# Kernel tuning notes

Hardware: AMD Instinct MI355X
Metric: run time of the kernel (lower is better)

Reference implementation:

```python
import jax, jax.numpy as jnp
import numpy as np

N_NODES = 100000
N_EDGES = 1600000
NODE_FEATURES = 6
H_EMBED = 64
D = 32
OUT_DIM = 1


def _mlp(x, W1, b1, W2, b2):
    h = jnp.tanh(x @ W1 + b1)
    return jnp.tanh(h @ W2 + b2)


def _gcn_conv(h, W, b, src, dst, n_nodes):
    # PyG GCNConv: linear (no bias) -> add self-loops -> sym-normalized scatter-add -> +bias
    hw = h @ W  # [N, D]
    loop = jnp.arange(n_nodes, dtype=src.dtype)
    row = jnp.concatenate([src, loop])  # sources
    col = jnp.concatenate([dst, loop])  # targets
    ones = jnp.ones(row.shape[0], dtype=hw.dtype)
    deg = jax.ops.segment_sum(ones, col, num_segments=n_nodes)
    dinv = jnp.where(deg > 0, jax.lax.rsqrt(deg), 0.0)
    norm = dinv[row] * dinv[col]  # [E+N]
    msg = hw[row] * norm[:, None]  # gather + scale
    out = jax.ops.segment_sum(msg, col, num_segments=n_nodes)
    return out + b


def setup_inputs() -> dict:
    key = jax.random.key(0)
    ks = jax.random.split(key, 16)
    x = jax.random.normal(ks[0], (N_NODES, NODE_FEATURES), dtype=jnp.float32)
    edge_index = jax.random.randint(ks[1], (2, N_EDGES), 0, N_NODES, dtype=jnp.int64)

    def lin(k, din, dout):
        bound = 1.0 / np.sqrt(din)
        kw, kb = jax.random.split(k)
        W = jax.random.uniform(kw, (din, dout), minval=-bound, maxval=bound, dtype=jnp.float32)
        b = jax.random.uniform(kb, (dout,), minval=-bound, maxval=bound, dtype=jnp.float32)
        return W, b

    We1, be1 = lin(ks[2], NODE_FEATURES, H_EMBED)
    We2, be2 = lin(ks[3], H_EMBED, D)
    Wg1, bg1 = lin(ks[4], D, D)
    Wg2, bg2 = lin(ks[5], D, D)
    Wp1, bp1 = lin(ks[6], D, D)
    Wp2, bp2 = lin(ks[7], D, OUT_DIM)
    return {
        "x": x, "edge_index": edge_index,
        "We1": We1, "be1": be1, "We2": We2, "be2": be2,
        "Wg1": Wg1, "bg1": bg1, "Wg2": Wg2, "bg2": bg2,
        "Wp1": Wp1, "bp1": bp1, "Wp2": Wp2, "bp2": bp2,
    }


def reference(x, edge_index, We1, be1, We2, be2, Wg1, bg1, Wg2, bg2, Wp1, bp1, Wp2, bp2):
    n = x.shape[0]
    src, dst = edge_index[0], edge_index[1]
    h = _mlp(x, We1, be1, We2, be2)            # [N, 32]
    h = jax.nn.relu(_gcn_conv(h, Wg1, bg1, src, dst, n))  # dropout = identity (eval)
    h = jax.nn.relu(_gcn_conv(h, Wg2, bg2, src, dst, n))
    return _mlp(h, Wp1, bp1, Wp2, bp2)         # [N, 1]
```

## Files before the change

kernel.cpp:

```cpp
#include <hip/hip_runtime.h>
#include <hip/hip_fp16.h>

#define NN 100000
#define NE 1600000
#define NPB 128
#define NBUCK ((NN + NPB - 1) / NPB)
#define CAP 4096
#define PBLOCKS 128
#define PTPB 1024
#define EPB (NE / PBLOCKS)
#define DUMMY 100000u
#define SENT 0xFFFFFFFFu
#define GBLK 2048
#define GWAVES (GBLK * 4)

__global__ __launch_bounds__(PTPB) void part_kernel(const int* __restrict__ src,
                                                    const int* __restrict__ dst,
                                                    unsigned int* __restrict__ bcount,
                                                    unsigned int* __restrict__ packed) {
    __shared__ unsigned int lcnt[NBUCK];
    __shared__ unsigned int lcur[NBUCK];
    __shared__ unsigned int lend[NBUCK];
    for (int i = threadIdx.x; i < NBUCK; i += PTPB) lcnt[i] = 0u;
    __syncthreads();
    int e0 = blockIdx.x * EPB;
    for (int e = e0 + threadIdx.x; e < e0 + EPB; e += PTPB)
        atomicAdd(&lcnt[((unsigned)dst[e]) >> 7], 1u);
    __syncthreads();
    for (int i = threadIdx.x; i < NBUCK; i += PTPB) {
        unsigned int c = lcnt[i];
        unsigned int rc = (c + 15u) & ~15u;
        unsigned int base = rc ? atomicAdd(&bcount[i], rc) : 0u;
        lcur[i] = base;
        lend[i] = base + rc;
    }
    __syncthreads();
    for (int e = e0 + threadIdx.x; e < e0 + EPB; e += PTPB) {
        unsigned int d = (unsigned)dst[e];
        unsigned int b = d >> 7;
        unsigned int pos = atomicAdd(&lcur[b], 1u);
        packed[(size_t)b * CAP + pos] = ((d & 127u) << 17) | (unsigned)src[e];
    }
    __syncthreads();
    for (int i = threadIdx.x; i < NBUCK; i += PTPB)
        for (unsigned int j = lcur[i]; j < lend[i]; j++)
            packed[(size_t)i * CAP + j] = SENT;
}

__global__ __launch_bounds__(256) void sort_kernel(const unsigned int* __restrict__ bcount,
                                                   unsigned int* __restrict__ packed,
                                                   unsigned int* __restrict__ rsd,
                                                   float* __restrict__ dinv) {
    __shared__ unsigned int lraw[CAP];
    __shared__ unsigned int lsort[CAP];
    __shared__ unsigned int cnt[NPB];
    __shared__ unsigned int ps[NPB];
    __shared__ unsigned int cur[NPB];
    __shared__ unsigned int ntot;
    int b = blockIdx.x;
    int tid = threadIdx.x;
    if (tid < NPB) cnt[tid] = 0u;
    __syncthreads();
    unsigned int n = bcount[b];
    unsigned int* pk = packed + (size_t)b * CAP;
    for (unsigned int i = tid; i < n; i += 256) {
        unsigned int p = pk[i];
        lraw[i] = p;
        if (p != SENT) atomicAdd(&cnt[p >> 17], 1u);
    }
    __syncthreads();
    if (tid < NPB) ps[tid] = (cnt[tid] + 15u) & ~15u;
    __syncthreads();
    for (int off = 1; off < NPB; off <<= 1) {
        unsigned int t = (tid < NPB && tid >= off) ? ps[tid - off] : 0u;
        __syncthreads();
        if (tid < NPB) ps[tid] += t;
        __syncthreads();
    }
    if (tid == NPB - 1) ntot = ps[NPB - 1];
    __syncthreads();
    unsigned int np = ntot;
    for (unsigned int i = tid; i < np; i += 256) lsort[i] = DUMMY;
    if (tid < NPB) cur[tid] = ps[tid] - ((cnt[tid] + 15u) & ~15u);
    __syncthreads();
    for (unsigned int i = tid; i < n; i += 256) {
        unsigned int p = lraw[i];
        if (p != SENT) {
            unsigned int pos = atomicAdd(&cur[p >> 17], 1u);
            lsort[pos] = p & 0x1FFFFu;
        }
    }
    __syncthreads();
    for (unsigned int i = tid; i < np; i += 256) pk[i] = lsort[i];
    if (tid < NPB) {
        int node = b * NPB + tid;
        if (node < NN) {
            unsigned int c = cnt[tid];
            unsigned int pc = (c + 15u) & ~15u;
            unsigned int rs = (unsigned int)(b * CAP) + ps[tid] - pc;
            rsd[node] = rs | ((pc >> 4) << 22);
            dinv[node] = rsqrtf((float)c + 1.0f);
        }
    }
}

__global__ __launch_bounds__(256) void embed_kernel(
    const float* __restrict__ x, const float* __restrict__ We1, const float* __restrict__ be1,
    const float* __restrict__ We2, const float* __restrict__ be2, const float* __restrict__ Wg1,
    const float* __restrict__ dinv, __half* __restrict__ hws1, __half* __restrict__ hws2) {
    __shared__ float sWe1[6 * 64];
    __shared__ float sbe1[64];
    __shared__ float sWe2[64 * 32];
    __shared__ float sbe2[32];
    __shared__ float sWg1[32 * 32];
    for (int i = threadIdx.x; i < 6 * 64; i += 256) sWe1[i] = We1[i];
    for (int i = threadIdx.x; i < 64; i += 256) sbe1[i] = be1[i];
    for (int i = threadIdx.x; i < 64 * 32; i += 256) sWe2[i] = We2[i];
    for (int i = threadIdx.x; i < 32; i += 256) sbe2[i] = be2[i];
    for (int i = threadIdx.x; i < 32 * 32; i += 256) sWg1[i] = Wg1[i];
    __syncthreads();

    int node = blockIdx.x * 256 + threadIdx.x;
    if (node > NN) return;
    if (node == NN) {
        for (int j = 0; j < 32; j++) {
            hws1[(size_t)NN * 32 + j] = __float2half(0.f);
            hws2[(size_t)NN * 32 + j] = __float2half(0.f);
        }
        return;
    }

    float xv[6];
#pragma unroll
    for (int k = 0; k < 6; k++) xv[k] = x[node * 6 + k];

    float h1[64];
#pragma unroll
    for (int j = 0; j < 64; j++) {
        float a = sbe1[j];
#pragma unroll
        for (int k = 0; k < 6; k++) a += xv[k] * sWe1[k * 64 + j];
        h1[j] = tanhf(a);
    }

    float h[32];
#pragma unroll 4
    for (int j = 0; j < 32; j++) {
        float a = sbe2[j];
#pragma unroll
        for (int k = 0; k < 64; k++) a += h1[k] * sWe2[k * 32 + j];
        h[j] = tanhf(a);
    }

    float di = dinv[node];
    __half* o = hws1 + (size_t)node * 32;
#pragma unroll 4
    for (int j = 0; j < 32; j++) {
        float a = 0.f;
#pragma unroll
        for (int k = 0; k < 32; k++) a += h[k] * sWg1[k * 32 + j];
        o[j] = __float2half(a * di);
    }
}

__global__ __launch_bounds__(256) void gather1_kernel(
    const unsigned int* __restrict__ sorted, const unsigned int* __restrict__ rsd,
    const float* __restrict__ dinv, const __half* __restrict__ hws1,
    const float* __restrict__ bg1, const float* __restrict__ Wg2,
    __half* __restrict__ hws2) {
    int lane = threadIdx.x & 63;
    int g = lane >> 4;
    int p = lane & 15;
    int f = lane & 31;
    float wreg[32];
#pragma unroll
    for (int k = 0; k < 32; k++) wreg[k] = Wg2[k * 32 + f];
    float bf = bg1[f];
    int wave = (blockIdx.x * 256 + threadIdx.x) >> 6;
    const __half2* H = (const __half2*)hws1;
    for (int node = wave; node < NN; node += GWAVES) {
        unsigned int r = rsd[node];
        unsigned int base = r & 0x3FFFFFu;
        unsigned int d = (r >> 22) << 4;
        float ax = 0.f, ay = 0.f;
        for (unsigned int k = g; k < d; k += 16) {
            unsigned int s0 = sorted[base + k];
            unsigned int s1 = sorted[base + k + 4];
            unsigned int s2 = sorted[base + k + 8];
            unsigned int s3 = sorted[base + k + 12];
            float2 v0 = __half22float2(H[(size_t)s0 * 16 + p]);
            float2 v1 = __half22float2(H[(size_t)s1 * 16 + p]);
            float2 v2 = __half22float2(H[(size_t)s2 * 16 + p]);
            float2 v3 = __half22float2(H[(size_t)s3 * 16 + p]);
            ax += (v0.x + v1.x) + (v2.x + v3.x);
            ay += (v0.y + v1.y) + (v2.y + v3.y);
        }
        ax += __shfl_xor(ax, 16); ay += __shfl_xor(ay, 16);
        ax += __shfl_xor(ax, 32); ay += __shfl_xor(ay, 32);
        float2 sv = __half22float2(H[(size_t)node * 16 + p]);
        ax += sv.x; ay += sv.y;
        float ae = __shfl(ax, f >> 1);
        float ao = __shfl(ay, f >> 1);
        float av = (f & 1) ? ao : ae;
        float di = dinv[node];
        float h = di * av + bf;
        h = h > 0.f ? h : 0.f;
        float o = 0.f;
#pragma unroll
        for (int k = 0; k < 32; k++) o += __shfl(h, k) * wreg[k];
        if (lane < 32) hws2[(size_t)node * 32 + f] = __float2half(o * di);
    }
}

__global__ __launch_bounds__(256) void gather2_kernel(
    const unsigned int* __restrict__ sorted, const unsigned int* __restrict__ rsd,
    const float* __restrict__ dinv, const __half* __restrict__ hws2,
    const float* __restrict__ bg2, const float* __restrict__ Wp1,
    const float* __restrict__ bp1, const float* __restrict__ Wp2,
    const float* __restrict__ bp2, float* __restrict__ out) {
    int lane = threadIdx.x & 63;
    int g = lane >> 4;
    int p = lane & 15;
    int f = lane & 31;
    float wreg[32];
#pragma unroll
    for (int k = 0; k < 32; k++) wreg[k] = Wp1[k * 32 + f];
    float bgf = bg2[f];
    float b1f = bp1[f];
    float w2f = Wp2[f];
    float b2 = bp2[0];
    int wave = (blockIdx.x * 256 + threadIdx.x) >> 6;
    const __half2* H = (const __half2*)hws2;
    for (int node = wave; node < NN; node += GWAVES) {
        unsigned int r = rsd[node];
        unsigned int base = r & 0x3FFFFFu;
        unsigned int d = (r >> 22) << 4;
        float ax = 0.f, ay = 0.f;
        for (unsigned int k = g; k < d; k += 16) {
            unsigned int s0 = sorted[base + k];
            unsigned int s1 = sorted[base + k + 4];
            unsigned int s2 = sorted[base + k + 8];
            unsigned int s3 = sorted[base + k + 12];
            float2 v0 = __half22float2(H[(size_t)s0 * 16 + p]);
            float2 v1 = __half22float2(H[(size_t)s1 * 16 + p]);
            float2 v2 = __half22float2(H[(size_t)s2 * 16 + p]);
            float2 v3 = __half22float2(H[(size_t)s3 * 16 + p]);
            ax += (v0.x + v1.x) + (v2.x + v3.x);
            ay += (v0.y + v1.y) + (v2.y + v3.y);
        }
        ax += __shfl_xor(ax, 16); ay += __shfl_xor(ay, 16);
        ax += __shfl_xor(ax, 32); ay += __shfl_xor(ay, 32);
        float2 sv = __half22float2(H[(size_t)node * 16 + p]);
        ax += sv.x; ay += sv.y;
        float ae = __shfl(ax, f >> 1);
        float ao = __shfl(ay, f >> 1);
        float av = (f & 1) ? ao : ae;
        float di = dinv[node];
        float h = di * av + bgf;
        h = h > 0.f ? h : 0.f;
        float pre = b1f;
#pragma unroll
        for (int k = 0; k < 32; k++) pre += __shfl(h, k) * wreg[k];
        float t = tanhf(pre) * w2f;
#pragma unroll
        for (int off = 1; off < 32; off <<= 1) t += __shfl_xor(t, off);
        if (lane == 0) out[node] = tanhf(t + b2);
    }
}

extern "C" void kernel_launch(void* const* d_in, const int* in_sizes, int n_in,
                              void* d_out, int out_size, void* d_ws, size_t ws_size,
                              hipStream_t stream) {
    const float* x = (const float*)d_in[0];
    const int* edge = (const int*)d_in[1];
    const int* src = edge;
    const int* dst = edge + NE;
    const float* We1 = (const float*)d_in[2];
    const float* be1 = (const float*)d_in[3];
    const float* We2 = (const float*)d_in[4];
    const float* be2 = (const float*)d_in[5];
    const float* Wg1 = (const float*)d_in[6];
    const float* bg1 = (const float*)d_in[7];
    const float* Wg2 = (const float*)d_in[8];
    const float* bg2 = (const float*)d_in[9];
    const float* Wp1 = (const float*)d_in[10];
    const float* bp1 = (const float*)d_in[11];
    const float* Wp2 = (const float*)d_in[12];
    const float* bp2 = (const float*)d_in[13];
    float* out = (float*)d_out;

    unsigned int* bcount = (unsigned int*)d_ws;
    float* dinv = (float*)d_ws + 1024;
    unsigned int* rsd = (unsigned int*)d_ws + 1024 + NN;
    unsigned int* packed = (unsigned int*)d_ws + 1024 + 2 * NN;
    __half* hws1 = (__half*)((unsigned int*)d_ws + 1024 + 2 * NN + NBUCK * CAP);
    __half* hws2 = hws1 + (size_t)(NN + 1) * 32;

    hipMemsetAsync(bcount, 0, 1024 * sizeof(unsigned int), stream);

    int gridN = (NN + 256) / 256;

    part_kernel<<<PBLOCKS, PTPB, 0, stream>>>(src, dst, bcount, packed);
    sort_kernel<<<NBUCK, 256, 0, stream>>>(bcount, packed, rsd, dinv);
    embed_kernel<<<gridN, 256, 0, stream>>>(x, We1, be1, We2, be2, Wg1, dinv, hws1, hws2);
    gather1_kernel<<<GBLK, 256, 0, stream>>>(packed, rsd, dinv, hws1, bg1, Wg2, hws2);
    gather2_kernel<<<GBLK, 256, 0, stream>>>(packed, rsd, dinv, hws2, bg2, Wp1, bp1, Wp2, bp2, out);
}
```

Before: 278.9 us.

## Map each node to a half-wave and reduce neighbor padding to eight

Each 64-lane wave now serves two nodes: every 32-lane half-wave handles one node's aggregation and the dense 32x32 transform. Per-node neighbor lists are padded to multiples of 8 instead of 16, so fewer dummy rows are gathered. Neighbor indices are loaded four at a time with one uint4 load. Partition and sort block counts, thread counts and the bucket capacity are retuned to fit. In exchange, each node has less memory-level parallelism per gather, the shuffles now use width 32, and the packed buffer needs more workspace.

Measured after the change: 246.0 us. 11.8% less time.

```diff
diff --git a/kernel.cpp b/kernel.cpp
--- a/kernel.cpp
+++ b/kernel.cpp
@@ -5,14 +5,14 @@
 #define NE 1600000
 #define NPB 128
 #define NBUCK ((NN + NPB - 1) / NPB)
-#define CAP 4096
-#define PBLOCKS 128
-#define PTPB 1024
+#define CAP 4608
+#define PBLOCKS 256
+#define PTPB 512
 #define EPB (NE / PBLOCKS)
 #define DUMMY 100000u
 #define SENT 0xFFFFFFFFu
-#define GBLK 2048
-#define GWAVES (GBLK * 4)
+#define GBLK 4096
+#define NSLOT (GBLK * 8)
 
 __global__ __launch_bounds__(PTPB) void part_kernel(const int* __restrict__ src,
                                                     const int* __restrict__ dst,
@@ -29,7 +29,7 @@
     __syncthreads();
     for (int i = threadIdx.x; i < NBUCK; i += PTPB) {
         unsigned int c = lcnt[i];
-        unsigned int rc = (c + 15u) & ~15u;
+        unsigned int rc = (c + 7u) & ~7u;
         unsigned int base = rc ? atomicAdd(&bcount[i], rc) : 0u;
         lcur[i] = base;
         lend[i] = base + rc;
@@ -47,7 +47,7 @@
             packed[(size_t)i * CAP + j] = SENT;
 }
 
-__global__ __launch_bounds__(256) void sort_kernel(const unsigned int* __restrict__ bcount,
+__global__ __launch_bounds__(512) void sort_kernel(const unsigned int* __restrict__ bcount,
                                                    unsigned int* __restrict__ packed,
                                                    unsigned int* __restrict__ rsd,
                                                    float* __restrict__ dinv) {
@@ -63,13 +63,13 @@
     __syncthreads();
     unsigned int n = bcount[b];
     unsigned int* pk = packed + (size_t)b * CAP;
-    for (unsigned int i = tid; i < n; i += 256) {
+    for (unsigned int i = tid; i < n; i += 512) {
         unsigned int p = pk[i];
         lraw[i] = p;
         if (p != SENT) atomicAdd(&cnt[p >> 17], 1u);
     }
     __syncthreads();
-    if (tid < NPB) ps[tid] = (cnt[tid] + 15u) & ~15u;
+    if (tid < NPB) ps[tid] = (cnt[tid] + 7u) & ~7u;
     __syncthreads();
     for (int off = 1; off < NPB; off <<= 1) {
         unsigned int t = (tid < NPB && tid >= off) ? ps[tid - off] : 0u;
@@ -80,10 +80,10 @@
     if (tid == NPB - 1) ntot = ps[NPB - 1];
     __syncthreads();
     unsigned int np = ntot;
-    for (unsigned int i = tid; i < np; i += 256) lsort[i] = DUMMY;
-    if (tid < NPB) cur[tid] = ps[tid] - ((cnt[tid] + 15u) & ~15u);
-    __syncthreads();
-    for (unsigned int i = tid; i < n; i += 256) {
+    for (unsigned int i = tid; i < np; i += 512) lsort[i] = DUMMY;
+    if (tid < NPB) cur[tid] = ps[tid] - ((cnt[tid] + 7u) & ~7u);
+    __syncthreads();
+    for (unsigned int i = tid; i < n; i += 512) {
         unsigned int p = lraw[i];
         if (p != SENT) {
             unsigned int pos = atomicAdd(&cur[p >> 17], 1u);
@@ -91,14 +91,14 @@
         }
     }
     __syncthreads();
-    for (unsigned int i = tid; i < np; i += 256) pk[i] = lsort[i];
+    for (unsigned int i = tid; i < np; i += 512) pk[i] = lsort[i];
     if (tid < NPB) {
         int node = b * NPB + tid;
         if (node < NN) {
             unsigned int c = cnt[tid];
-            unsigned int pc = (c + 15u) & ~15u;
+            unsigned int pc = (c + 7u) & ~7u;
             unsigned int rs = (unsigned int)(b * CAP) + ps[tid] - pc;
-            rsd[node] = rs | ((pc >> 4) << 22);
+            rsd[node] = rs | ((pc >> 3) << 22);
             dinv[node] = rsqrtf((float)c + 1.0f);
         }
     }
@@ -168,47 +168,43 @@
     const float* __restrict__ dinv, const __half* __restrict__ hws1,
     const float* __restrict__ bg1, const float* __restrict__ Wg2,
     __half* __restrict__ hws2) {
-    int lane = threadIdx.x & 63;
+    int lane = threadIdx.x & 31;
     int g = lane >> 4;
     int p = lane & 15;
-    int f = lane & 31;
+    int f = lane;
     float wreg[32];
 #pragma unroll
     for (int k = 0; k < 32; k++) wreg[k] = Wg2[k * 32 + f];
     float bf = bg1[f];
-    int wave = (blockIdx.x * 256 + threadIdx.x) >> 6;
+    int slot = (blockIdx.x * 256 + threadIdx.x) >> 5;
     const __half2* H = (const __half2*)hws1;
-    for (int node = wave; node < NN; node += GWAVES) {
+    for (int node = slot; node < NN; node += NSLOT) {
         unsigned int r = rsd[node];
         unsigned int base = r & 0x3FFFFFu;
-        unsigned int d = (r >> 22) << 4;
+        unsigned int d = (r >> 22) << 3;
         float ax = 0.f, ay = 0.f;
-        for (unsigned int k = g; k < d; k += 16) {
-            unsigned int s0 = sorted[base + k];
-            unsigned int s1 = sorted[base + k + 4];
-            unsigned int s2 = sorted[base + k + 8];
-            unsigned int s3 = sorted[base + k + 12];
-            float2 v0 = __half22float2(H[(size_t)s0 * 16 + p]);
-            float2 v1 = __half22float2(H[(size_t)s1 * 16 + p]);
-            float2 v2 = __half22float2(H[(size_t)s2 * 16 + p]);
-            float2 v3 = __half22float2(H[(size_t)s3 * 16 + p]);
+        for (unsigned int k = g * 4; k < d; k += 8) {
+            uint4 s4 = *reinterpret_cast<const uint4*>(sorted + base + k);
+            float2 v0 = __half22float2(H[(size_t)s4.x * 16 + p]);
+            float2 v1 = __half22float2(H[(size_t)s4.y * 16 + p]);
+            float2 v2 = __half22float2(H[(size_t)s4.z * 16 + p]);
+            float2 v3 = __half22float2(H[(size_t)s4.w * 16 + p]);
             ax += (v0.x + v1.x) + (v2.x + v3.x);
             ay += (v0.y + v1.y) + (v2.y + v3.y);
         }
         ax += __shfl_xor(ax, 16); ay += __shfl_xor(ay, 16);
-        ax += __shfl_xor(ax, 32); ay += __shfl_xor(ay, 32);
         float2 sv = __half22float2(H[(size_t)node * 16 + p]);
         ax += sv.x; ay += sv.y;
-        float ae = __shfl(ax, f >> 1);
-        float ao = __shfl(ay, f >> 1);
+        float ae = __shfl(ax, f >> 1, 32);
+        float ao = __shfl(ay, f >> 1, 32);
         float av = (f & 1) ? ao : ae;
         float di = dinv[node];
         float h = di * av + bf;
         h = h > 0.f ? h : 0.f;
         float o = 0.f;
 #pragma unroll
-        for (int k = 0; k < 32; k++) o += __shfl(h, k) * wreg[k];
-        if (lane < 32) hws2[(size_t)node * 32 + f] = __float2half(o * di);
+        for (int k = 0; k < 32; k++) o += __shfl(h, k, 32) * wreg[k];
+        hws2[(size_t)node * 32 + f] = __float2half(o * di);
     }
 }
 
@@ -218,10 +214,10 @@
     const float* __restrict__ bg2, const float* __restrict__ Wp1,
     const float* __restrict__ bp1, const float* __restrict__ Wp2,
     const float* __restrict__ bp2, float* __restrict__ out) {
-    int lane = threadIdx.x & 63;
+    int lane = threadIdx.x & 31;
     int g = lane >> 4;
     int p = lane & 15;
-    int f = lane & 31;
+    int f = lane;
     float wreg[32];
 #pragma unroll
     for (int k = 0; k < 32; k++) wreg[k] = Wp1[k * 32 + f];
@@ -229,38 +225,34 @@
     float b1f = bp1[f];
     float w2f = Wp2[f];
     float b2 = bp2[0];
-    int wave = (blockIdx.x * 256 + threadIdx.x) >> 6;
+    int slot = (blockIdx.x * 256 + threadIdx.x) >> 5;
     const __half2* H = (const __half2*)hws2;
-    for (int node = wave; node < NN; node += GWAVES) {
+    for (int node = slot; node < NN; node += NSLOT) {
         unsigned int r = rsd[node];
         unsigned int base = r & 0x3FFFFFu;
-        unsigned int d = (r >> 22) << 4;
+        unsigned int d = (r >> 22) << 3;
         float ax = 0.f, ay = 0.f;
-        for (unsigned int k = g; k < d; k += 16) {
-            unsigned int s0 = sorted[base + k];
-            unsigned int s1 = sorted[base + k + 4];
-            unsigned int s2 = sorted[base + k + 8];
-            unsigned int s3 = sorted[base + k + 12];
-            float2 v0 = __half22float2(H[(size_t)s0 * 16 + p]);
-            float2 v1 = __half22float2(H[(size_t)s1 * 16 + p]);
-            float2 v2 = __half22float2(H[(size_t)s2 * 16 + p]);
-            float2 v3 = __half22float2(H[(size_t)s3 * 16 + p]);
+        for (unsigned int k = g * 4; k < d; k += 8) {
+            uint4 s4 = *reinterpret_cast<const uint4*>(sorted + base + k);
+            float2 v0 = __half22float2(H[(size_t)s4.x * 16 + p]);
+            float2 v1 = __half22float2(H[(size_t)s4.y * 16 + p]);
+            float2 v2 = __half22float2(H[(size_t)s4.z * 16 + p]);
+            float2 v3 = __half22float2(H[(size_t)s4.w * 16 + p]);
             ax += (v0.x + v1.x) + (v2.x + v3.x);
             ay += (v0.y + v1.y) + (v2.y + v3.y);
         }
         ax += __shfl_xor(ax, 16); ay += __shfl_xor(ay, 16);
-        ax += __shfl_xor(ax, 32); ay += __shfl_xor(ay, 32);
         float2 sv = __half22float2(H[(size_t)node * 16 + p]);
         ax += sv.x; ay += sv.y;
-        float ae = __shfl(ax, f >> 1);
-        float ao = __shfl(ay, f >> 1);
+        float ae = __shfl(ax, f >> 1, 32);
+        float ao = __shfl(ay, f >> 1, 32);
         float av = (f & 1) ? ao : ae;
         float di = dinv[node];
         float h = di * av + bgf;
         h = h > 0.f ? h : 0.f;
         float pre = b1f;
 #pragma unroll
-        for (int k = 0; k < 32; k++) pre += __shfl(h, k) * wreg[k];
+        for (int k = 0; k < 32; k++) pre += __shfl(h, k, 32) * wreg[k];
         float t = tanhf(pre) * w2f;
 #pragma unroll
         for (int off = 1; off < 32; off <<= 1) t += __shfl_xor(t, off);
@@ -301,7 +293,7 @@
     int gridN = (NN + 256) / 256;
 
     part_kernel<<<PBLOCKS, PTPB, 0, stream>>>(src, dst, bcount, packed);
-    sort_kernel<<<NBUCK, 256, 0, stream>>>(bcount, packed, rsd, dinv);
+    sort_kernel<<<NBUCK, 512, 0, stream>>>(bcount, packed, rsd, dinv);
     embed_kernel<<<gridN, 256, 0, stream>>>(x, We1, be1, We2, be2, Wg1, dinv, hws1, hws2);
     gather1_kernel<<<GBLK, 256, 0, stream>>>(packed, rsd, dinv, hws1, bg1, Wg2, hws2);
     gather2_kernel<<<GBLK, 256, 0, stream>>>(packed, rsd, dinv, hws2, bg2, Wp1, bp1, Wp2, bp2, out);
```
